# Performance work log

Hardware: AMD Instinct MI355X
Metric: run time of the kernel (lower is better)

## Reference

```python
import jax, jax.numpy as jnp
import numpy as np

N_EMBED = 256
N_HEAD = 8
HEAD = N_EMBED // N_HEAD
LN_EPS = 1e-5


def _layernorm(x, g, b):
    mu = jnp.mean(x, axis=-1, keepdims=True)
    var = jnp.mean(jnp.square(x - mu), axis=-1, keepdims=True)
    return (x - mu) * jax.lax.rsqrt(var + LN_EPS) * g + b


def setup_inputs() -> dict:
    key = jax.random.key(0)
    ks = jax.random.split(key, 12)
    B, T, C, H, D = 16, 1024, N_EMBED, N_HEAD, HEAD
    s = C ** -0.5
    return {
        "x": jax.random.normal(ks[0], (B, T, C), jnp.float32),
        "wq": jax.random.normal(ks[1], (H, C, D), jnp.float32) * s,
        "wk": jax.random.normal(ks[2], (H, C, D), jnp.float32) * s,
        "wv": jax.random.normal(ks[3], (H, C, D), jnp.float32) * s,
        "w_proj": jax.random.normal(ks[4], (C, C), jnp.float32) * s,
        "b_proj": jnp.zeros((C,), jnp.float32),
        "w1": jax.random.normal(ks[5], (C, 4 * C), jnp.float32) * s,
        "b1": jnp.zeros((4 * C,), jnp.float32),
        "w2": jax.random.normal(ks[6], (4 * C, C), jnp.float32) * (4 * C) ** -0.5,
        "b2": jnp.zeros((C,), jnp.float32),
        "ln1_g": jnp.ones((C,), jnp.float32),
        "ln1_b": jnp.zeros((C,), jnp.float32),
        "ln2_g": jnp.ones((C,), jnp.float32),
        "ln2_b": jnp.zeros((C,), jnp.float32),
    }


def reference(x, wq, wk, wv, w_proj, b_proj, w1, b1, w2, b2,
              ln1_g, ln1_b, ln2_g, ln2_b):
    B, T, C = x.shape
    # --- multi-head causal self-attention on ln1(x) ---
    h = _layernorm(x, ln1_g, ln1_b)
    q = jnp.einsum('btc,hcd->bhtd', h, wq)
    k = jnp.einsum('btc,hcd->bhtd', h, wk)
    v = jnp.einsum('btc,hcd->bhtd', h, wv)
    # NOTE: original scales by n_embed**-0.5 (C of input), not head_size
    wei = jnp.einsum('bhtd,bhsd->bhts', q, k) * (C ** -0.5)
    causal = jnp.tril(jnp.ones((T, T), bool))
    wei = jnp.where(causal, wei, -jnp.inf)
    wei = jax.nn.softmax(wei, axis=-1)
    att = jnp.einsum('bhts,bhsd->bhtd', wei, v)
    att = att.transpose(0, 2, 1, 3).reshape(B, T, C)  # concat heads
    x = x + att @ w_proj + b_proj
    # --- feedforward on ln2(x) ---
    h2 = _layernorm(x, ln2_g, ln2_b)
    f = jax.nn.relu(h2 @ w1 + b1) @ w2 + b2
    return x + f
```

## Files before the change

### kernel.cpp

```cpp
#include <hip/hip_runtime.h>


typedef unsigned short u16;
typedef unsigned int u32;
typedef __attribute__((ext_vector_type(8))) short short8v;
typedef __attribute__((ext_vector_type(4))) float float4v;

__device__ __forceinline__ float b2f(u16 u) { union { u32 i; float f; } v; v.i = (u32)u << 16; return v.f; }
__device__ __forceinline__ float lo2f(u32 u) { union { u32 i; float f; } v; v.i = u << 16; return v.f; }
__device__ __forceinline__ float hi2f(u32 u) { union { u32 i; float f; } v; v.i = u & 0xffff0000u; return v.f; }
__device__ __forceinline__ u16 f2b(float f) {
    union { float f; u32 i; } v; v.f = f;
    u32 r = v.i + 0x7fffu + ((v.i >> 16) & 1u);
    return (u16)(r >> 16);
}
__device__ __forceinline__ u32 pk2_rtz(float a, float b) {
    return (__float_as_uint(a) >> 16) | (__float_as_uint(b) & 0xffff0000u);
}
__device__ __forceinline__ void async_cp16(const u16* g, u16* l) {
    __builtin_amdgcn_global_load_lds((const __attribute__((address_space(1))) void*)g,
                                     (__attribute__((address_space(3))) void*)l, 16, 0, 0);
}

__global__ __launch_bounds__(256) void prep_ln1(const float* __restrict__ wq,
                                                const float* __restrict__ wk,
                                                const float* __restrict__ wv,
                                                const float* __restrict__ wp,
                                                const float* __restrict__ w1,
                                                const float* __restrict__ w2,
                                                const float* __restrict__ x,
                                                const float* __restrict__ g1,
                                                const float* __restrict__ be1,
                                                u16* __restrict__ wqkvT,
                                                u16* __restrict__ wpT,
                                                u16* __restrict__ w1T,
                                                u16* __restrict__ w2T,
                                                u16* __restrict__ hout) {
    __shared__ u16 tile[64][65];
    int bid = blockIdx.x, tid = threadIdx.x;
    if (bid < 768) {
        int i = bid * 256 + tid;
        int n = i >> 8, k = i & 255;
        int which = n >> 8, nn = n & 255;
        const float* w = which == 0 ? wq : (which == 1 ? wk : wv);
        float v = w[((nn >> 5) * 256 + k) * 32 + (nn & 31)];
        if (which == 0) v *= 0.09016844f;
        wqkvT[i] = f2b(v);
    } else if (bid < 912) {
        const float* src; u16* dst; int K, N, t;
        if (bid < 784)      { src = wp; dst = wpT; K = 256;  N = 256;  t = bid - 768; }
        else if (bid < 848) { src = w1; dst = w1T; K = 256;  N = 1024; t = bid - 784; }
        else                { src = w2; dst = w2T; K = 1024; N = 256;  t = bid - 848; }
        int ntn = N >> 6;
        int k0 = (t / ntn) << 6, n0 = (t % ntn) << 6;
        int lane = tid & 63, wrow = tid >> 6;
        #pragma unroll
        for (int r = 0; r < 16; r++) {
            int k = wrow * 16 + r;
            tile[k][lane] = f2b(src[(size_t)(k0 + k) * N + n0 + lane]);
        }
        __syncthreads();
        #pragma unroll
        for (int r = 0; r < 16; r++) {
            int n = wrow * 16 + r;
            dst[(size_t)(n0 + n) * K + k0 + lane] = tile[lane][n];
        }
    } else {
        int row = (bid - 912) * 4 + (tid >> 6);
        int lane = tid & 63;
        float4 xv = *(const float4*)(x + (size_t)row * 256 + lane * 4);
        float v0 = xv.x, v1 = xv.y, v2 = xv.z, v3 = xv.w;
        float s = v0 + v1 + v2 + v3;
        #pragma unroll
        for (int m = 32; m; m >>= 1) s += __shfl_xor(s, m);
        float mu = s * 0.00390625f;
        float d0 = v0 - mu, d1 = v1 - mu, d2 = v2 - mu, d3 = v3 - mu;
        float ss = d0 * d0 + d1 * d1 + d2 * d2 + d3 * d3;
        #pragma unroll
        for (int m = 32; m; m >>= 1) ss += __shfl_xor(ss, m);
        float rs = rsqrtf(ss * 0.00390625f + 1e-5f);
        float4 g = *(const float4*)(g1 + lane * 4);
        float4 b = *(const float4*)(be1 + lane * 4);
        uint2 r;
        r.x = (u32)f2b(d0 * rs * g.x + b.x) | ((u32)f2b(d1 * rs * g.y + b.y) << 16);
        r.y = (u32)f2b(d2 * rs * g.z + b.z) | ((u32)f2b(d3 * rs * g.w + b.w) << 16);
        *(uint2*)(hout + (size_t)row * 256 + lane * 4) = r;
    }
}

template<bool HASBIAS, bool RELU, bool QKV>
__global__ __launch_bounds__(256) void gemm128(const u16* __restrict__ A,
                                               const u16* __restrict__ Bt,
                                               const float* __restrict__ bias,
                                               u16* __restrict__ out,
                                               u16* __restrict__ vout,
                                               int M, int N, int K) {
    __shared__ __align__(16) u16 SH[17408];
    u16* As = SH;
    u16* Bs = SH + 128 * 64;
    const int tid = threadIdx.x, lane = tid & 63, w = tid >> 6;
    const int m0 = blockIdx.x * 128, n0 = blockIdx.y * 128;
    const int wm = (w & 1) * 64, wn = (w >> 1) * 64;
    const int fm = lane & 15, q = lane >> 4;

    float4v acc[4][4];
    #pragma unroll
    for (int i = 0; i < 4; i++)
        #pragma unroll
        for (int j = 0; j < 4; j++) acc[i][j] = (float4v){0.f, 0.f, 0.f, 0.f};

    const int kset = ((lane & 7) ^ (lane >> 3)) * 8;
    const u16* Ag = A  + (size_t)(m0 + w * 32 + (lane >> 3)) * K + kset;
    const u16* Bg = Bt + (size_t)(n0 + w * 32 + (lane >> 3)) * K + kset;
    u16* Asw = As + (w * 32) * 64;
    u16* Bsw = Bs + (w * 32) * 64;

    const int sw = fm & 7;
    for (int k0 = 0; k0 < K; k0 += 64) {
        __syncthreads();
        #pragma unroll
        for (int c = 0; c < 4; c++) {
            async_cp16(Ag + (size_t)c * 8 * K + k0, Asw + c * 8 * 64);
            async_cp16(Bg + (size_t)c * 8 * K + k0, Bsw + c * 8 * 64);
        }
        __syncthreads();
        #pragma unroll
        for (int kk = 0; kk < 64; kk += 32) {
            const int slot = (((kk >> 3) + q) ^ sw) * 8;
            short8v af[4], bf[4];
            #pragma unroll
            for (int mi = 0; mi < 4; mi++)
                af[mi] = *(const short8v*)&As[(wm + mi * 16 + fm) * 64 + slot];
            #pragma unroll
            for (int ni = 0; ni < 4; ni++)
                bf[ni] = *(const short8v*)&Bs[(wn + ni * 16 + fm) * 64 + slot];
            #pragma unroll
            for (int mi = 0; mi < 4; mi++)
                #pragma unroll
                for (int ni = 0; ni < 4; ni++)
                    acc[mi][ni] = __builtin_amdgcn_mfma_f32_16x16x32_bf16(
                        bf[ni], af[mi], acc[mi][ni], 0, 0, 0);
        }
    }

    if (QKV && n0 >= 512) {
        __syncthreads();
        #pragma unroll
        for (int mi = 0; mi < 4; mi++) {
            int ml = wm + mi * 16 + fm;
            #pragma unroll
            for (int ni = 0; ni < 4; ni++) {
                int nl = wn + ni * 16 + q * 4;
                #pragma unroll
                for (int r = 0; r < 4; r++)
                    SH[(nl + r) * 136 + ml] = f2b(acc[mi][ni][r]);
            }
        }
        __syncthreads();
        int r = tid & 127, c = (tid >> 7) << 6;
        int hd = (n0 - 512) + r;
        int b = m0 >> 10, t0 = m0 & 1023;
        u16* dst = vout + (size_t)(b * 256 + hd) * 1024 + t0 + c;
        const u16* srcT = SH + r * 136 + c;
        #pragma unroll
        for (int i = 0; i < 8; i++)
            *(uint4*)(dst + i * 8) = *(const uint4*)(srcT + i * 8);
        return;
    }

    #pragma unroll
    for (int mi = 0; mi < 4; mi++) {
        int row = m0 + wm + mi * 16 + fm;
        #pragma unroll
        for (int ni = 0; ni < 4; ni++) {
            int nb = n0 + wn + ni * 16 + q * 4;
            float v0 = acc[mi][ni][0], v1 = acc[mi][ni][1],
                  v2 = acc[mi][ni][2], v3 = acc[mi][ni][3];
            if (HASBIAS) {
                float4 bv = *(const float4*)&bias[nb];
                v0 += bv.x; v1 += bv.y; v2 += bv.z; v3 += bv.w;
            }
            if (RELU) {
                v0 = fmaxf(v0, 0.f); v1 = fmaxf(v1, 0.f);
                v2 = fmaxf(v2, 0.f); v3 = fmaxf(v3, 0.f);
            }
            size_t idx = (size_t)row * N + nb;
            uint2 ov;
            ov.x = (u32)f2b(v0) | ((u32)f2b(v1) << 16);
            ov.y = (u32)f2b(v2) | ((u32)f2b(v3) << 16);
            *(uint2*)&out[idx] = ov;
        }
    }
}

__global__ __launch_bounds__(256) void gemm64(const u16* __restrict__ A,
                                              const u16* __restrict__ Bt,
                                              const float* __restrict__ bias,
                                              const u16* __restrict__ resid,
                                              float* __restrict__ out,
                                              int M, int N, int K) {
    __shared__ __align__(16) u16 As[64 * 64];
    __shared__ __align__(16) u16 Bs[128 * 64];
    const int tid = threadIdx.x, lane = tid & 63, w = tid >> 6;
    const int m0 = blockIdx.x * 64, n0 = blockIdx.y * 128;
    const int wm = (w & 1) * 32, wn = (w >> 1) * 64;
    const int fm = lane & 15, q = lane >> 4;

    float4v acc[2][4];
    #pragma unroll
    for (int i = 0; i < 2; i++)
        #pragma unroll
        for (int j = 0; j < 4; j++) acc[i][j] = (float4v){0.f, 0.f, 0.f, 0.f};

    const int kset = ((lane & 7) ^ (lane >> 3)) * 8;
    const u16* Ag = A  + (size_t)(m0 + w * 16 + (lane >> 3)) * K + kset;
    const u16* Bg = Bt + (size_t)(n0 + w * 32 + (lane >> 3)) * K + kset;
    u16* Asw = As + (w * 16) * 64;
    u16* Bsw = Bs + (w * 32) * 64;

    const int sw = fm & 7;
    for (int k0 = 0; k0 < K; k0 += 64) {
        __syncthreads();
        #pragma unroll
        for (int c = 0; c < 2; c++)
            async_cp16(Ag + (size_t)c * 8 * K + k0, Asw + c * 8 * 64);
        #pragma unroll
        for (int c = 0; c < 4; c++)
            async_cp16(Bg + (size_t)c * 8 * K + k0, Bsw + c * 8 * 64);
        __syncthreads();
        #pragma unroll
        for (int kk = 0; kk < 64; kk += 32) {
            const int slot = (((kk >> 3) + q) ^ sw) * 8;
            short8v af[2], bf[4];
            #pragma unroll
            for (int mi = 0; mi < 2; mi++)
                af[mi] = *(const short8v*)&As[(wm + mi * 16 + fm) * 64 + slot];
            #pragma unroll
            for (int ni = 0; ni < 4; ni++)
                bf[ni] = *(const short8v*)&Bs[(wn + ni * 16 + fm) * 64 + slot];
            #pragma unroll
            for (int mi = 0; mi < 2; mi++)
                #pragma unroll
                for (int ni = 0; ni < 4; ni++)
                    acc[mi][ni] = __builtin_amdgcn_mfma_f32_16x16x32_bf16(
                        bf[ni], af[mi], acc[mi][ni], 0, 0, 0);
        }
    }

    #pragma unroll
    for (int mi = 0; mi < 2; mi++) {
        int row = m0 + wm + mi * 16 + fm;
        #pragma unroll
        for (int ni = 0; ni < 4; ni++) {
            int nb = n0 + wn + ni * 16 + q * 4;
            size_t idx = (size_t)row * N + nb;
            float4 bv = *(const float4*)&bias[nb];
            uint2 rv = *(const uint2*)&resid[idx];
            float v0 = acc[mi][ni][0] + bv.x + lo2f(rv.x);
            float v1 = acc[mi][ni][1] + bv.y + hi2f(rv.x);
            float v2 = acc[mi][ni][2] + bv.z + lo2f(rv.y);
            float v3 = acc[mi][ni][3] + bv.w + hi2f(rv.y);
            *(float4*)&out[idx] = (float4){v0, v1, v2, v3};
        }
    }
}

__global__ __launch_bounds__(256) void proj_ln2(const u16* __restrict__ att,
                                                const u16* __restrict__ wpT,
                                                const float* __restrict__ bp,
                                                const float* __restrict__ x,
                                                const float* __restrict__ g2,
                                                const float* __restrict__ be2,
                                                u16* __restrict__ x2b,
                                                u16* __restrict__ h2) {
    __shared__ __align__(16) u16 As[32 * 64];
    __shared__ __align__(16) u16 Bs[256 * 64];
    __shared__ float gs[256], bs[256], bps[256];
    __shared__ float ps[4][16], pq[4][16];
    const int tid = threadIdx.x, lane = tid & 63, w = tid >> 6;
    const int m0 = blockIdx.x * 32;
    const int wm = (w & 1) * 16, wn = (w >> 1) * 128;
    const int fm = lane & 15, q = lane >> 4;

    gs[tid] = g2[tid]; bs[tid] = be2[tid]; bps[tid] = bp[tid];

    float4v acc[8];
    #pragma unroll
    for (int i = 0; i < 8; i++) acc[i] = (float4v){0.f, 0.f, 0.f, 0.f};

    const int kset = ((lane & 7) ^ (lane >> 3)) * 8;
    const u16* Ag = att + (size_t)(m0 + w * 8 + (lane >> 3)) * 256 + kset;
    const u16* Bg = wpT + (size_t)(w * 64 + (lane >> 3)) * 256 + kset;
    u16* Asw = As + (w * 8) * 64;
    u16* Bsw = Bs + (w * 64) * 64;

    const int sw = fm & 7;
    for (int k0 = 0; k0 < 256; k0 += 64) {
        __syncthreads();
        async_cp16(Ag + k0, Asw);
        #pragma unroll
        for (int c = 0; c < 8; c++)
            async_cp16(Bg + (size_t)c * 8 * 256 + k0, Bsw + c * 8 * 64);
        __syncthreads();
        #pragma unroll
        for (int kk = 0; kk < 64; kk += 32) {
            const int slot = (((kk >> 3) + q) ^ sw) * 8;
            short8v af = *(const short8v*)&As[(wm + fm) * 64 + slot];
            #pragma unroll
            for (int ni = 0; ni < 8; ni++) {
                short8v bf = *(const short8v*)&Bs[(wn + ni * 16 + fm) * 64 + slot];
                acc[ni] = __builtin_amdgcn_mfma_f32_16x16x32_bf16(bf, af, acc[ni], 0, 0, 0);
            }
        }
    }

    int m = m0 + wm + fm;
    float v[8][4];
    float s = 0.f, sq = 0.f;
    #pragma unroll
    for (int ni = 0; ni < 8; ni++) {
        int nb = wn + ni * 16 + q * 4;
        float4 xv = *(const float4*)(x + (size_t)m * 256 + nb);
        float4 bv = *(const float4*)&bps[nb];
        #pragma unroll
        for (int r = 0; r < 4; r++) {
            float t = acc[ni][r] + (&bv.x)[r] + (&xv.x)[r];
            v[ni][r] = t;
            s += t; sq += t * t;
        }
    }
    s += __shfl_xor(s, 16);  s += __shfl_xor(s, 32);
    sq += __shfl_xor(sq, 16); sq += __shfl_xor(sq, 32);
    if (q == 0) { ps[w][fm] = s; pq[w][fm] = sq; }
    __syncthreads();
    s = ps[w][fm] + ps[w ^ 2][fm];
    sq = pq[w][fm] + pq[w ^ 2][fm];
    float mu = s * 0.00390625f;
    float rs = rsqrtf(sq * 0.00390625f - mu * mu + 1e-5f);
    #pragma unroll
    for (int ni = 0; ni < 8; ni++) {
        int nb = wn + ni * 16 + q * 4;
        size_t idx = (size_t)m * 256 + nb;
        float4 gv = *(const float4*)&gs[nb];
        float4 bv = *(const float4*)&bs[nb];
        uint2 xo, ho;
        xo.x = (u32)f2b(v[ni][0]) | ((u32)f2b(v[ni][1]) << 16);
        xo.y = (u32)f2b(v[ni][2]) | ((u32)f2b(v[ni][3]) << 16);
        float h0 = (v[ni][0] - mu) * rs * gv.x + bv.x;
        float h1 = (v[ni][1] - mu) * rs * gv.y + bv.y;
        float h2v = (v[ni][2] - mu) * rs * gv.z + bv.z;
        float h3 = (v[ni][3] - mu) * rs * gv.w + bv.w;
        ho.x = (u32)f2b(h0) | ((u32)f2b(h1) << 16);
        ho.y = (u32)f2b(h2v) | ((u32)f2b(h3) << 16);
        *(uint2*)&x2b[idx] = xo;
        *(uint2*)&h2[idx] = ho;
    }
}

__global__ __launch_bounds__(256) void attn_mfma(const u16* __restrict__ qk,
                                                 const u16* __restrict__ vtg,
                                                 u16* __restrict__ att) {
    const int T = 1024;
    int jj = (blockIdx.x + (blockIdx.y >> 3)) & 7;
    int b = blockIdx.y >> 3, hh = blockIdx.y & 7;
    int tid = threadIdx.x;
    int lane = tid & 63, w = tid >> 6;
    int fm = lane & 15, q = lane >> 4;

    __shared__ __align__(16) u16 Ks[64][72];
    __shared__ __align__(16) u16 Vt[32][72];
    __shared__ __align__(16) u16 Pl[4][16][72];

    size_t base = (size_t)b * T * 512;
    const u16* kb = qk + base + 256 + hh * 32;
    const u16* vt = vtg + (size_t)((b * 8 + hh) * 32) * 1024;
    const int krow = tid >> 2, kcol = (tid & 3) * 8;
    const int vd = tid >> 3, vs = (tid & 7) * 8;

    int qa0 = jj * 64, qb0 = (15 - jj) * 64;
    int tqa = qa0 + w * 16 + fm, tqb = qb0 + w * 16 + fm;
    short8v qfa = *(const short8v*)(qk + base + (size_t)tqa * 512 + hh * 32 + q * 8);
    short8v qfb = *(const short8v*)(qk + base + (size_t)tqb * 512 + hh * 32 + q * 8);
    float4v oa0 = {0.f, 0.f, 0.f, 0.f}, oa1 = {0.f, 0.f, 0.f, 0.f};
    float4v ob0 = {0.f, 0.f, 0.f, 0.f}, ob1 = {0.f, 0.f, 0.f, 0.f};
    float la = 0.f, lb = 0.f;
    int wqa = qa0 + w * 16, wqb = qb0 + w * 16;
    int nIter = 16 - jj;

    uint4 kreg = *(const uint4*)(kb + (size_t)krow * 512 + kcol);
    uint4 vreg = *(const uint4*)(vt + (size_t)vd * 1024 + vs);

    for (int it = 0; it < nIter; ++it) {
        int s0 = it << 6;
        __syncthreads();
        *(uint4*)&Ks[krow][kcol] = kreg;
        *(uint4*)&Vt[vd][vs] = vreg;
        __syncthreads();
        if (it + 1 < nIter) {
            int ns0 = s0 + 64;
            kreg = *(const uint4*)(kb + (size_t)(ns0 + krow) * 512 + kcol);
            vreg = *(const uint4*)(vt + (size_t)vd * 1024 + ns0 + vs);
        }
        short8v kf0 = *(const short8v*)&Ks[fm][q * 8];
        short8v kf1 = *(const short8v*)&Ks[16 + fm][q * 8];
        short8v kf2 = *(const short8v*)&Ks[32 + fm][q * 8];
        short8v kf3 = *(const short8v*)&Ks[48 + fm][q * 8];
        short8v vf00 = *(const short8v*)&Vt[fm][q * 8];
        short8v vf01 = *(const short8v*)&Vt[fm][32 + q * 8];
        short8v vf10 = *(const short8v*)&Vt[16 + fm][q * 8];
        short8v vf11 = *(const short8v*)&Vt[16 + fm][32 + q * 8];
        float4v z = {0.f, 0.f, 0.f, 0.f};

        #pragma unroll
        for (int t2 = 0; t2 < 2; t2++) {
            int wq0 = t2 ? wqa : wqb;
            if (s0 >= wq0 + 16) continue;
            int tq = t2 ? tqa : tqb;
            short8v qf = t2 ? qfa : qfb;
            float4v s_0 = __builtin_amdgcn_mfma_f32_16x16x32_bf16(kf0, qf, z, 0, 0, 0);
            float4v s_1 = __builtin_amdgcn_mfma_f32_16x16x32_bf16(kf1, qf, z, 0, 0, 0);
            float4v s_2 = __builtin_amdgcn_mfma_f32_16x16x32_bf16(kf2, qf, z, 0, 0, 0);
            float4v s_3 = __builtin_amdgcn_mfma_f32_16x16x32_bf16(kf3, qf, z, 0, 0, 0);
            float p[16];
            #pragma unroll
            for (int r = 0; r < 4; r++) {
                p[r] = exp2f(s_0[r]); p[4 + r] = exp2f(s_1[r]);
                p[8 + r] = exp2f(s_2[r]); p[12 + r] = exp2f(s_3[r]);
            }
            if (s0 + 63 > wq0) {
                int sb = s0 + q * 4;
                #pragma unroll
                for (int c = 0; c < 4; c++)
                    #pragma unroll
                    for (int r = 0; r < 4; r++)
                        if (sb + c * 16 + r > tq) p[c * 4 + r] = 0.f;
            }
            float rsum = 0.f;
            #pragma unroll
            for (int i = 0; i < 16; i++) rsum += p[i];
            rsum += __shfl_xor(rsum, 16);
            rsum += __shfl_xor(rsum, 32);
            if (t2) la += rsum; else lb += rsum;

            #pragma unroll
            for (int c = 0; c < 4; c++) {
                uint2 pp;
                pp.x = pk2_rtz(p[c * 4 + 0], p[c * 4 + 1]);
                pp.y = pk2_rtz(p[c * 4 + 2], p[c * 4 + 3]);
                *(uint2*)&Pl[w][fm][c * 16 + q * 4] = pp;
            }
            short8v pf0 = *(const short8v*)&Pl[w][fm][q * 8];
            short8v pf1 = *(const short8v*)&Pl[w][fm][32 + q * 8];
            if (t2) {
                oa0 = __builtin_amdgcn_mfma_f32_16x16x32_bf16(vf00, pf0, oa0, 0, 0, 0);
                oa0 = __builtin_amdgcn_mfma_f32_16x16x32_bf16(vf01, pf1, oa0, 0, 0, 0);
                oa1 = __builtin_amdgcn_mfma_f32_16x16x32_bf16(vf10, pf0, oa1, 0, 0, 0);
                oa1 = __builtin_amdgcn_mfma_f32_16x16x32_bf16(vf11, pf1, oa1, 0, 0, 0);
            } else {
                ob0 = __builtin_amdgcn_mfma_f32_16x16x32_bf16(vf00, pf0, ob0, 0, 0, 0);
                ob0 = __builtin_amdgcn_mfma_f32_16x16x32_bf16(vf01, pf1, ob0, 0, 0, 0);
                ob1 = __builtin_amdgcn_mfma_f32_16x16x32_bf16(vf10, pf0, ob1, 0, 0, 0);
                ob1 = __builtin_amdgcn_mfma_f32_16x16x32_bf16(vf11, pf1, ob1, 0, 0, 0);
            }
        }
    }

    #pragma unroll
    for (int t2 = 0; t2 < 2; t2++) {
        float inv = 1.f / (t2 ? la : lb);
        float4v o0 = t2 ? oa0 : ob0, o1 = t2 ? oa1 : ob1;
        int tq = t2 ? tqa : tqb;
        uint2 r0, r1;
        r0.x = (u32)f2b(o0[0] * inv) | ((u32)f2b(o0[1] * inv) << 16);
        r0.y = (u32)f2b(o0[2] * inv) | ((u32)f2b(o0[3] * inv) << 16);
        r1.x = (u32)f2b(o1[0] * inv) | ((u32)f2b(o1[1] * inv) << 16);
        r1.y = (u32)f2b(o1[2] * inv) | ((u32)f2b(o1[3] * inv) << 16);
        size_t o = (size_t)(b * T + tq) * 256 + hh * 32;
        *(uint2*)(att + o + q * 4) = r0;
        *(uint2*)(att + o + 16 + q * 4) = r1;
    }
}

extern "C" void kernel_launch(void* const* d_in, const int* in_sizes, int n_in,
                              void* d_out, int out_size, void* d_ws, size_t ws_size,
                              hipStream_t stream) {
    const int BT = 16 * 1024;
    const float* x      = (const float*)d_in[0];
    const float* wq     = (const float*)d_in[1];
    const float* wk     = (const float*)d_in[2];
    const float* wv     = (const float*)d_in[3];
    const float* w_proj = (const float*)d_in[4];
    const float* b_proj = (const float*)d_in[5];
    const float* w1     = (const float*)d_in[6];
    const float* b1     = (const float*)d_in[7];
    const float* w2     = (const float*)d_in[8];
    const float* b2     = (const float*)d_in[9];
    const float* ln1_g  = (const float*)d_in[10];
    const float* ln1_b  = (const float*)d_in[11];
    const float* ln2_g  = (const float*)d_in[12];
    const float* ln2_b  = (const float*)d_in[13];

    char* ws = (char*)d_ws;
    const size_t MB = 1024 * 1024;
    u16*  x2b   = (u16*)(ws + 0);
    u16*  hbuf  = (u16*)(ws + 8 * MB);
    u16*  qk    = (u16*)(ws + 16 * MB);
    u16*  vtg   = (u16*)(ws + 32 * MB);
    u16*  mid   = (u16*)(ws + 16 * MB);
    u16*  wqkvT = (u16*)(ws + 48 * MB);
    u16*  wpT   = (u16*)(ws + 48 * MB + 0x60000);
    u16*  w1T   = (u16*)(ws + 48 * MB + 0x80000);
    u16*  w2T   = (u16*)(ws + 48 * MB + 0x100000);

    prep_ln1<<<5008, 256, 0, stream>>>(wq, wk, wv, w_proj, w1, w2, x, ln1_g, ln1_b,
                                       wqkvT, wpT, w1T, w2T, hbuf);
    gemm128<false, false, true><<<dim3(128, 6), 256, 0, stream>>>(
        hbuf, wqkvT, nullptr, qk, vtg, BT, 512, 256);
    attn_mfma<<<dim3(8, 128), 256, 0, stream>>>(qk, vtg, hbuf);
    proj_ln2<<<512, 256, 0, stream>>>(hbuf, wpT, b_proj, x, ln2_g, ln2_b, x2b, hbuf);
    gemm128<true, true, false><<<dim3(128, 8), 256, 0, stream>>>(
        hbuf, w1T, b1, mid, nullptr, BT, 1024, 256);
    gemm64<<<dim3(256, 2), 256, 0, stream>>>(
        mid, w2T, b2, x2b, (float*)d_out, BT, 256, 1024);
}
```

Baseline: 196.1 us.

## Fuse FFN up-projection, ReLU and down-projection into one kernel

Replaces the separate w1 GEMM (writing a 16Kx1024 bf16 intermediate to global memory) and the w2 GEMM with a single kernel. Each block handles 32 rows and walks the hidden dimension in 256-wide chunks, keeping the ReLU output in swizzled LDS before feeding it to the second GEMM. This removes one launch and the intermediate's global write and read. In exchange each block streams all of w1 and w2 through LDS with no double buffering, the tile is only 32 rows, and the grid is smaller.

```diff
diff --git a/kernel.cpp b/kernel.cpp
--- a/kernel.cpp
+++ b/kernel.cpp
@@ -193,73 +193,110 @@
     }
 }
 
-__global__ __launch_bounds__(256) void gemm64(const u16* __restrict__ A,
-                                              const u16* __restrict__ Bt,
-                                              const float* __restrict__ bias,
-                                              const u16* __restrict__ resid,
-                                              float* __restrict__ out,
-                                              int M, int N, int K) {
-    __shared__ __align__(16) u16 As[64 * 64];
-    __shared__ __align__(16) u16 Bs[128 * 64];
+__global__ __launch_bounds__(256, 2) void ffn_fused(const u16* __restrict__ h2,
+                                                    const u16* __restrict__ w1T,
+                                                    const float* __restrict__ b1,
+                                                    const u16* __restrict__ w2T,
+                                                    const float* __restrict__ b2,
+                                                    const u16* __restrict__ x2b,
+                                                    float* __restrict__ out) {
+    __shared__ __align__(16) u16 SH[32768];
+    u16* As = SH;
+    u16* Bs = SH + 8192;
+    u16* Ms = SH + 24576;
     const int tid = threadIdx.x, lane = tid & 63, w = tid >> 6;
-    const int m0 = blockIdx.x * 64, n0 = blockIdx.y * 128;
-    const int wm = (w & 1) * 32, wn = (w >> 1) * 64;
+    const int m0 = blockIdx.x * 32;
+    const int wm = (w & 1) * 16;
+    const int wn = (w >> 1) * 128;
     const int fm = lane & 15, q = lane >> 4;
-
-    float4v acc[2][4];
-    #pragma unroll
-    for (int i = 0; i < 2; i++)
-        #pragma unroll
-        for (int j = 0; j < 4; j++) acc[i][j] = (float4v){0.f, 0.f, 0.f, 0.f};
-
+    const int sw = fm & 7;
     const int kset = ((lane & 7) ^ (lane >> 3)) * 8;
-    const u16* Ag = A  + (size_t)(m0 + w * 16 + (lane >> 3)) * K + kset;
-    const u16* Bg = Bt + (size_t)(n0 + w * 32 + (lane >> 3)) * K + kset;
-    u16* Asw = As + (w * 16) * 64;
-    u16* Bsw = Bs + (w * 32) * 64;
-
-    const int sw = fm & 7;
-    for (int k0 = 0; k0 < K; k0 += 64) {
-        __syncthreads();
-        #pragma unroll
-        for (int c = 0; c < 2; c++)
-            async_cp16(Ag + (size_t)c * 8 * K + k0, Asw + c * 8 * 64);
-        #pragma unroll
-        for (int c = 0; c < 4; c++)
-            async_cp16(Bg + (size_t)c * 8 * K + k0, Bsw + c * 8 * 64);
-        __syncthreads();
-        #pragma unroll
-        for (int kk = 0; kk < 64; kk += 32) {
-            const int slot = (((kk >> 3) + q) ^ sw) * 8;
-            short8v af[2], bf[4];
-            #pragma unroll
-            for (int mi = 0; mi < 2; mi++)
-                af[mi] = *(const short8v*)&As[(wm + mi * 16 + fm) * 64 + slot];
-            #pragma unroll
-            for (int ni = 0; ni < 4; ni++)
-                bf[ni] = *(const short8v*)&Bs[(wn + ni * 16 + fm) * 64 + slot];
-            #pragma unroll
-            for (int mi = 0; mi < 2; mi++)
+
+    const u16* Ag = h2 + (size_t)(m0 + w * 8 + (lane >> 3)) * 256 + kset;
+    #pragma unroll
+    for (int kc = 0; kc < 4; kc++)
+        async_cp16(Ag + kc * 64, As + kc * 2048 + w * 512);
+
+    const u16* Bg1 = w1T + (size_t)(w * 64 + (lane >> 3)) * 256 + kset;
+    const u16* Bg2 = w2T + (size_t)(w * 64 + (lane >> 3)) * 1024 + kset;
+    u16* Bsw = Bs + (w * 64) * 64;
+
+    float4v acc2[8];
+    #pragma unroll
+    for (int i = 0; i < 8; i++) acc2[i] = (float4v){0.f, 0.f, 0.f, 0.f};
+
+    for (int nch = 0; nch < 4; nch++) {
+        float4v acc1[8];
+        #pragma unroll
+        for (int i = 0; i < 8; i++) acc1[i] = (float4v){0.f, 0.f, 0.f, 0.f};
+        const u16* src1 = Bg1 + (size_t)nch * 256 * 256;
+        for (int kc = 0; kc < 4; kc++) {
+            __syncthreads();
+            #pragma unroll
+            for (int c = 0; c < 8; c++)
+                async_cp16(src1 + (size_t)c * 8 * 256 + kc * 64, Bsw + c * 8 * 64);
+            __syncthreads();
+            #pragma unroll
+            for (int kk = 0; kk < 64; kk += 32) {
+                const int slot = (((kk >> 3) + q) ^ sw) * 8;
+                short8v af = *(const short8v*)&As[kc * 2048 + (wm + fm) * 64 + slot];
                 #pragma unroll
-                for (int ni = 0; ni < 4; ni++)
-                    acc[mi][ni] = __builtin_amdgcn_mfma_f32_16x16x32_bf16(
-                        bf[ni], af[mi], acc[mi][ni], 0, 0, 0);
-        }
-    }
-
-    #pragma unroll
-    for (int mi = 0; mi < 2; mi++) {
-        int row = m0 + wm + mi * 16 + fm;
-        #pragma unroll
-        for (int ni = 0; ni < 4; ni++) {
-            int nb = n0 + wn + ni * 16 + q * 4;
-            size_t idx = (size_t)row * N + nb;
-            float4 bv = *(const float4*)&bias[nb];
-            uint2 rv = *(const uint2*)&resid[idx];
-            float v0 = acc[mi][ni][0] + bv.x + lo2f(rv.x);
-            float v1 = acc[mi][ni][1] + bv.y + hi2f(rv.x);
-            float v2 = acc[mi][ni][2] + bv.z + lo2f(rv.y);
-            float v3 = acc[mi][ni][3] + bv.w + hi2f(rv.y);
+                for (int ni = 0; ni < 8; ni++) {
+                    short8v bf = *(const short8v*)&Bs[(wn + ni * 16 + fm) * 64 + slot];
+                    acc1[ni] = __builtin_amdgcn_mfma_f32_16x16x32_bf16(bf, af, acc1[ni], 0, 0, 0);
+                }
+            }
+        }
+        {
+            int row = wm + fm;
+            #pragma unroll
+            for (int ni = 0; ni < 8; ni++) {
+                int c = wn + ni * 16 + q * 4;
+                float4 bv = *(const float4*)&b1[nch * 256 + c];
+                float v0 = fmaxf(acc1[ni][0] + bv.x, 0.f);
+                float v1 = fmaxf(acc1[ni][1] + bv.y, 0.f);
+                float v2 = fmaxf(acc1[ni][2] + bv.z, 0.f);
+                float v3 = fmaxf(acc1[ni][3] + bv.w, 0.f);
+                int kc = c >> 6, cc = c & 63;
+                int g = cc >> 3, p = cc & 7;
+                uint2 pp;
+                pp.x = (u32)f2b(v0) | ((u32)f2b(v1) << 16);
+                pp.y = (u32)f2b(v2) | ((u32)f2b(v3) << 16);
+                *(uint2*)&Ms[kc * 2048 + row * 64 + ((g ^ (row & 7)) * 8) + p] = pp;
+            }
+        }
+        const u16* src2 = Bg2 + nch * 256;
+        for (int kc = 0; kc < 4; kc++) {
+            __syncthreads();
+            #pragma unroll
+            for (int c = 0; c < 8; c++)
+                async_cp16(src2 + (size_t)c * 8 * 1024 + kc * 64, Bsw + c * 8 * 64);
+            __syncthreads();
+            #pragma unroll
+            for (int kk = 0; kk < 64; kk += 32) {
+                const int slot = (((kk >> 3) + q) ^ sw) * 8;
+                short8v af = *(const short8v*)&Ms[kc * 2048 + (wm + fm) * 64 + slot];
+                #pragma unroll
+                for (int ni = 0; ni < 8; ni++) {
+                    short8v bf = *(const short8v*)&Bs[(wn + ni * 16 + fm) * 64 + slot];
+                    acc2[ni] = __builtin_amdgcn_mfma_f32_16x16x32_bf16(bf, af, acc2[ni], 0, 0, 0);
+                }
+            }
+        }
+    }
+
+    {
+        int row = m0 + wm + fm;
+        #pragma unroll
+        for (int ni = 0; ni < 8; ni++) {
+            int nb = wn + ni * 16 + q * 4;
+            size_t idx = (size_t)row * 256 + nb;
+            float4 bv = *(const float4*)&b2[nb];
+            uint2 rv = *(const uint2*)&x2b[idx];
+            float v0 = acc2[ni][0] + bv.x + lo2f(rv.x);
+            float v1 = acc2[ni][1] + bv.y + hi2f(rv.x);
+            float v2 = acc2[ni][2] + bv.z + lo2f(rv.y);
+            float v3 = acc2[ni][3] + bv.w + hi2f(rv.y);
             *(float4*)&out[idx] = (float4){v0, v1, v2, v3};
         }
     }
@@ -506,7 +543,6 @@
     u16*  hbuf  = (u16*)(ws + 8 * MB);
     u16*  qk    = (u16*)(ws + 16 * MB);
     u16*  vtg   = (u16*)(ws + 32 * MB);
-    u16*  mid   = (u16*)(ws + 16 * MB);
     u16*  wqkvT = (u16*)(ws + 48 * MB);
     u16*  wpT   = (u16*)(ws + 48 * MB + 0x60000);
     u16*  w1T   = (u16*)(ws + 48 * MB + 0x80000);
@@ -518,8 +554,5 @@
         hbuf, wqkvT, nullptr, qk, vtg, BT, 512, 256);
     attn_mfma<<<dim3(8, 128), 256, 0, stream>>>(qk, vtg, hbuf);
     proj_ln2<<<512, 256, 0, stream>>>(hbuf, wpT, b_proj, x, ln2_g, ln2_b, x2b, hbuf);
-    gemm128<true, true, false><<<dim3(128, 8), 256, 0, stream>>>(
-        hbuf, w1T, b1, mid, nullptr, BT, 1024, 256);
-    gemm64<<<dim3(256, 2), 256, 0, stream>>>(
-        mid, w2T, b2, x2b, (float*)d_out, BT, 256, 1024);
-}
+    ffn_fused<<<512, 256, 0, stream>>>(hbuf, w1T, b1, w2T, b2, x2b, (float*)d_out);
+}
```

Result: no change. 196.3 us (+0.1%).
